# Optimization experiments

Measured on AMD Instinct MI355X. Metric: run time of the kernel, lower is better.

Reference implementation:

```python
import jax, jax.numpy as jnp
import numpy as np

B = 524288   # particles
H = 128      # hidden_size
E = 64       # embed_dim
NT = 512     # num trajectories
IN = 16 + 9 + E  # fc1 input dim = 89
EPS = 1e-6


def setup_inputs() -> dict:
    key = jax.random.key(0)
    ks = jax.random.split(key, 12)
    w = lambda k, shp, fan_in: (jax.random.normal(k, shp, dtype=jnp.float32)
                                / np.sqrt(fan_in).astype(np.float32))
    return {
        "F": jax.random.normal(ks[0], (B, 3, 3), dtype=jnp.float32),
        "C": jax.random.normal(ks[1], (B, 3, 3), dtype=jnp.float32),
        "traj_id": 7,
        "latent": jax.random.normal(ks[2], (NT, E), dtype=jnp.float32),
        "W1": w(ks[3], (IN, H), IN), "b1": jnp.zeros((H,), jnp.float32),
        "W2": w(ks[4], (H, H), H),   "b2": jnp.zeros((H,), jnp.float32),
        "W3": w(ks[5], (H, H), H),   "b3": jnp.zeros((H,), jnp.float32),
        "W4": w(ks[6], (H, H), H),   "b4": jnp.zeros((H,), jnp.float32),
        "W5": w(ks[7], (H, H), H),   "b5": jnp.zeros((H,), jnp.float32),
        "W6": w(ks[8], (H, H), H),   "b6": jnp.zeros((H,), jnp.float32),
        "W7": w(ks[9], (H, 9), H),   "b7": jnp.zeros((9,), jnp.float32),
    }


def _strain_features(F):
    # FFt: [B,3,3]; J = clamp(det F); J1 = clamp(F00); sigma: 3 singular values
    FFt = jnp.einsum('bij,bkj->bik', F, F)
    J = jnp.maximum(jnp.linalg.det(F), EPS)
    J1 = jnp.maximum(F[:, 0, 0], EPS)
    sigma = jnp.linalg.svd(F, compute_uv=False)  # descending, like torch.svd
    return jnp.concatenate([
        FFt.reshape(-1, 9),
        jnp.log(J)[:, None], sigma, J[:, None],
        jnp.log(J1)[:, None], J1[:, None],
    ], axis=-1)  # [B,16]


def reference(F, C, traj_id, latent,
              W1, b1, W2, b2, W3, b3, W4, b4, W5, b5, W6, b6, W7, b7):
    strain = _strain_features(F)                                   # [B,16]
    lat = jnp.broadcast_to(latent[traj_id], (F.shape[0], latent.shape[1]))
    x = jnp.concatenate([strain, C.reshape(-1, 9), lat], axis=-1)  # [B,89]
    g = lambda z: jax.nn.gelu(z, approximate=False)  # exact, matches torch GELU
    x = g(x @ W1 + b1)
    x = g(x @ W2 + b2)
    x = g(x @ W3 + b3)
    x = g(x @ W4 + b4)
    x = g(x @ W5 + b5)
    x = g(x @ W6 + b6)
    out = (x @ W7 + b7).reshape(-1, 3, 3)
    return 0.5 * (out + jnp.swapaxes(out, 1, 2))  # symmetric stress [B,3,3]
```

## Files before the change

### kernel.cpp

```cpp
#include <hip/hip_runtime.h>
#include <hip/hip_bf16.h>
#include <math.h>

#define BPART   524288
#define NBLK    (BPART / 256)
#define W7_OFF  98304
#define WB_N    102400
#define BIAS_N  800
#define PREP_N  (WB_N + BIAS_N)

typedef __bf16 bf16x8 __attribute__((ext_vector_type(8)));
typedef float  f32x16 __attribute__((ext_vector_type(16)));
typedef float  f32x4  __attribute__((ext_vector_type(4)));
typedef float  f32x2  __attribute__((ext_vector_type(2)));
typedef unsigned u32x4 __attribute__((ext_vector_type(4)));

#define MFMA __builtin_amdgcn_mfma_f32_32x32x16_bf16
#define UNROLL _Pragma("unroll")

__device__ __forceinline__ unsigned short f2bf(float f) {
  union { float f; unsigned u; } v; v.f = f;
  unsigned r = v.u + 0x7fffu + ((v.u >> 16) & 1u);
  return (unsigned short)(r >> 16);
}
__device__ __forceinline__ unsigned pack_bf16(float a, float b) {
  unsigned ua = __builtin_bit_cast(unsigned, a) + 0x8000u;
  unsigned ub = __builtin_bit_cast(unsigned, b) + 0x8000u;
  return __builtin_amdgcn_perm(ub, ua, 0x07060302u);
}

__device__ __forceinline__ int sigma(int n) {
  int c = ((n >> 5) << 2) | ((n >> 3) & 3);
  return ((c >> 1) << 4) | (((n >> 2) & 1) << 3) | ((c & 1) << 2) | (n & 3);
}

__device__ __forceinline__ f32x2 pk_mul(f32x2 a, f32x2 b) {
  f32x2 d; asm("v_pk_mul_f32 %0, %1, %2" : "=v"(d) : "v"(a), "v"(b)); return d;
}
__device__ __forceinline__ f32x2 pk_fma(f32x2 a, f32x2 b, f32x2 c) {
  f32x2 d; asm("v_pk_fma_f32 %0, %1, %2, %3" : "=v"(d) : "v"(a), "v"(b), "v"(c)); return d;
}
__device__ __forceinline__ f32x2 gelu2(f32x2 z) {
  const f32x2 c1 = {0.1029432f, 0.1029432f};
  const f32x2 c0 = {2.30220818f, 2.30220818f};
  f32x2 z2 = pk_mul(z, z);
  f32x2 t  = pk_fma(z2, c1, c0);
  f32x2 yp = pk_mul(z, t);
  float e0 = __builtin_amdgcn_exp2f(-yp.x);
  float e1 = __builtin_amdgcn_exp2f(-yp.y);
  float r0 = __builtin_amdgcn_rcpf(e0 + 1.0f);
  float r1 = __builtin_amdgcn_rcpf(e1 + 1.0f);
  f32x2 g; g.x = z.x * r0; g.y = z.y * r1;
  return g;
}
__device__ __forceinline__ void cp16(const void* g, void* l) {
  __builtin_amdgcn_global_load_lds(
      (const __attribute__((address_space(1))) void*)g,
      (__attribute__((address_space(3))) void*)l, 16, 0, 0);
}

__global__ void prep_weights(
    const float* __restrict__ W1, const float* __restrict__ W2,
    const float* __restrict__ W3, const float* __restrict__ W4,
    const float* __restrict__ W5, const float* __restrict__ W6,
    const float* __restrict__ W7,
    const float* __restrict__ b1, const float* __restrict__ b2,
    const float* __restrict__ b3, const float* __restrict__ b4,
    const float* __restrict__ b5, const float* __restrict__ b6,
    const float* __restrict__ b7,
    unsigned short* __restrict__ wsb, float* __restrict__ wsf)
{
  int idx = blockIdx.x * 256 + threadIdx.x;
  if (idx < WB_N) {
    unsigned short v = 0;
    if (idx < W7_OFF) {
      int l = idx >> 14;
      int o = idx & 16383;
      int n = o >> 7, e = o & 127;
      int k = (((e >> 3) ^ (n & 7)) << 3) | (e & 7);
      int sn = sigma(n);
      const float* W = (l==0)?W1:(l==1)?W2:(l==2)?W3:(l==3)?W4:(l==4)?W5:W6;
      float x = (l == 0) ? ((k < 89) ? W[k*128 + sn] : 0.0f)
                         : W[k*128 + sn];
      v = f2bf(x);
    } else {
      int o = idx - W7_OFF;
      int n = o >> 7, e = o & 127;
      int k = (((e >> 3) ^ (n & 7)) << 3) | (e & 7);
      int sn = sigma(n);
      v = (sn < 9) ? f2bf(W7[k*9 + sn]) : (unsigned short)0;
    }
    wsb[idx] = v;
  } else if (idx < PREP_N) {
    int r = idx - WB_N;
    float x;
    if (r < 768) {
      int l = r >> 7, n = r & 127;
      const float* bb = (l==0)?b1:(l==1)?b2:(l==2)?b3:(l==3)?b4:(l==4)?b5:b6;
      x = bb[sigma(n)];
    } else {
      int n = r - 768;
      int sn = sigma(n);
      x = (sn < 9) ? b7[sn] : 0.0f;
    }
    wsf[r] = x;
  }
}

#define MFMA_PAIR(WPTR, BLS, T0, NKK)                                         \
  UNROLL                                                                      \
  for (int kk = 0; kk < (NKK); ++kk) {                                        \
    bf16x8 x_ = __builtin_bit_cast(bf16x8, xw[kk]);                           \
    const int ch_ = ((2*kk + lk) ^ x7) << 3;                                  \
    UNROLL                                                                    \
    for (int t_ = 0; t_ < 2; ++t_) {                                          \
      const int tn_ = (T0) + t_;                                              \
      bf16x8 w_ = *(const bf16x8*)&(WPTR)[tn_*4096 + rb0 + ch_];              \
      if (kk == 0) {                                                          \
        f32x16 cf_;                                                           \
        UNROLL                                                                \
        for (int qq = 0; qq < 4; ++qq) {                                      \
          f32x4 b4_ = *(const f32x4*)&(BLS)[tn_*32 + qq*8 + lk*4];            \
          cf_[4*qq+0] = b4_[0]; cf_[4*qq+1] = b4_[1];                         \
          cf_[4*qq+2] = b4_[2]; cf_[4*qq+3] = b4_[3];                         \
        }                                                                     \
        acc[tn_] = MFMA(w_, x_, cf_, 0, 0, 0);                                \
      } else {                                                                \
        acc[tn_] = MFMA(w_, x_, acc[tn_], 0, 0, 0);                           \
      }                                                                       \
    }                                                                         \
  }

#define MFMA_LAYER(WPTR, NKK)                                                 \
  {                                                                           \
    const unsigned short* wp_ = (WPTR);                                       \
    const float* bls_ = (const float*)((const char*)wp_ + 32768);             \
    MFMA_PAIR(wp_, bls_, 0, NKK)                                              \
    MFMA_PAIR(wp_, bls_, 2, NKK)                                              \
  }

#define GELU_EPILOGUE                                                         \
  UNROLL                                                                      \
  for (int c = 0; c < 16; ++c) {                                              \
    const int tn_ = c >> 2, q_ = c & 3, t_ = c >> 1, h_ = c & 1;              \
    f32x2 za_, zb_;                                                           \
    za_.x = acc[tn_][4*q_+0]; za_.y = acc[tn_][4*q_+1];                       \
    zb_.x = acc[tn_][4*q_+2]; zb_.y = acc[tn_][4*q_+3];                       \
    f32x2 ga_ = gelu2(za_);                                                   \
    f32x2 gb_ = gelu2(zb_);                                                   \
    xw[t_][2*h_ + 0] = pack_bf16(ga_.x, ga_.y);                               \
    xw[t_][2*h_ + 1] = pack_bf16(gb_.x, gb_.y);                               \
  }

#define STAGE_W(LOFF, BUFIDX)                                                 \
  {                                                                           \
    const char* s_ = (const char*)(wst + (LOFF));                             \
    char* d_ = (char*)wbuf[BUFIDX];                                           \
    UNROLL                                                                    \
    for (int i_ = 0; i_ < 4; ++i_)                                            \
      cp16(s_ + i_*8192 + tid*16, d_ + i_*8192 + tid*16);                     \
  }
#define STAGE_B(BOFF, BUFIDX, NT)                                             \
  if (tid < (NT))                                                             \
    cp16((const char*)(wsf + (BOFF)) + tid*16,                                \
         (char*)wbuf[BUFIDX] + 32768 + tid*16);

__global__ __launch_bounds__(512, 4) void stress_mlp(
    const float* __restrict__ F, const float* __restrict__ Cmat,
    const int* __restrict__ traj, const float* __restrict__ latent,
    const unsigned short* __restrict__ wst, const float* __restrict__ wsf,
    float* __restrict__ out)
{
  __shared__ __align__(16) unsigned short wbuf[2][16384 + 256];

  const int tid  = threadIdx.x;
  const int lane = tid & 63;
  const int wid  = tid >> 6;
  const int lm   = lane & 31;
  const int lk   = lane >> 5;
  const int x7   = lm & 7;
  const int rb0  = lm << 7;
  const int pbase = (int)blockIdx.x << 8;
  const int p    = pbase + (wid << 5) + lm;

  STAGE_W(0, 0)
  STAGE_B(0, 0, 32)

  u32x4 xw[8];

  {
    const float* Fp = F + (size_t)p * 9;
    float f[9];
    UNROLL
    for (int i = 0; i < 9; ++i) f[i] = Fp[i];
    float fft[9];
    UNROLL
    for (int i = 0; i < 3; ++i)
      UNROLL
      for (int k = 0; k < 3; ++k)
        fft[i*3+k] = f[i*3]*f[k*3] + f[i*3+1]*f[k*3+1] + f[i*3+2]*f[k*3+2];
    const float* lat = latent + (size_t)traj[0] * 64;

    if (lk == 0) {
      xw[0][0] = pack_bf16(fft[0], fft[1]);
      xw[0][1] = pack_bf16(fft[2], fft[3]);
      xw[0][2] = pack_bf16(fft[4], fft[5]);
      xw[0][3] = pack_bf16(fft[6], fft[7]);
      const float* Cp = Cmat + (size_t)p * 9;
      UNROLL
      for (int i = 0; i < 4; ++i) xw[1][i] = pack_bf16(Cp[2*i], Cp[2*i+1]);
      UNROLL
      for (int t = 0; t < 4; ++t) {
        const float* lb = lat + 7 + 16*t;
        UNROLL
        for (int i = 0; i < 4; ++i) xw[2+t][i] = pack_bf16(lb[2*i], lb[2*i+1]);
      }
    } else {
      float det = f[0]*(f[4]*f[8]-f[5]*f[7]) - f[1]*(f[3]*f[8]-f[5]*f[6])
                + f[2]*(f[3]*f[7]-f[4]*f[6]);
      float J  = fmaxf(det, 1e-6f);
      float J1 = fmaxf(f[0], 1e-6f);
      float a00=fft[0], a01=fft[1], a02=fft[2], a11=fft[4], a12=fft[5], a22=fft[8];
      float q  = (a00+a11+a22) * (1.0f/3.0f);
      float d0 = a00-q, d1 = a11-q, d2 = a22-q;
      float p2 = d0*d0 + d1*d1 + d2*d2 + 2.0f*(a01*a01 + a02*a02 + a12*a12);
      float e0, e1, e2;
      if (p2 < 1e-14f) { e0 = e1 = e2 = q; }
      else {
        float pp  = sqrtf(p2 * (1.0f/6.0f));
        float inv = 1.0f / pp;
        float b00=d0*inv, b11=d1*inv, b22=d2*inv, b01=a01*inv, b02=a02*inv, b12=a12*inv;
        float detb = b00*(b11*b22-b12*b12) - b01*(b01*b22-b12*b02) + b02*(b01*b12-b11*b02);
        float rr = 0.5f * detb;
        rr = fminf(fmaxf(rr, -1.0f), 1.0f);
        float pr = acosf(rr) * (1.0f / (3.0f * 6.2831853071795864f));
        e0 = q + 2.0f*pp*__builtin_amdgcn_cosf(pr);
        e2 = q + 2.0f*pp*__builtin_amdgcn_cosf(pr + (1.0f/3.0f));
        e1 = 3.0f*q - e0 - e2;
      }
      float s0 = sqrtf(fmaxf(e0, 0.f));
      float s1 = sqrtf(fmaxf(e1, 0.f));
      float s2 = sqrtf(fmaxf(e2, 0.f));
      xw[0][0] = pack_bf16(fft[8], logf(J));
      xw[0][1] = pack_bf16(s0, s1);
      xw[0][2] = pack_bf16(s2, J);
      xw[0][3] = pack_bf16(logf(J1), J1);
      float c8 = Cmat[(size_t)p*9 + 8];
      xw[1][0] = pack_bf16(c8, lat[0]);
      xw[1][1] = pack_bf16(lat[1], lat[2]);
      xw[1][2] = pack_bf16(lat[3], lat[4]);
      xw[1][3] = pack_bf16(lat[5], lat[6]);
      UNROLL
      for (int t = 0; t < 3; ++t) {
        const float* lb = lat + 15 + 16*t;
        UNROLL
        for (int i = 0; i < 4; ++i) xw[2+t][i] = pack_bf16(lb[2*i], lb[2*i+1]);
      }
      xw[5][0] = pack_bf16(lat[63], 0.0f);
      xw[5][1] = 0u; xw[5][2] = 0u; xw[5][3] = 0u;
    }
  }

  f32x16 acc[4];

  __syncthreads();
  STAGE_W(1 << 14, 1) STAGE_B(128, 1, 32)
  MFMA_LAYER(wbuf[0], 6)
  GELU_EPILOGUE
  __syncthreads();

  STAGE_W(2 << 14, 0) STAGE_B(256, 0, 32)
  MFMA_LAYER(wbuf[1], 8)
  GELU_EPILOGUE
  __syncthreads();

  STAGE_W(3 << 14, 1) STAGE_B(384, 1, 32)
  MFMA_LAYER(wbuf[0], 8)
  GELU_EPILOGUE
  __syncthreads();

  STAGE_W(4 << 14, 0) STAGE_B(512, 0, 32)
  MFMA_LAYER(wbuf[1], 8)
  GELU_EPILOGUE
  __syncthreads();

  STAGE_W(5 << 14, 1) STAGE_B(640, 1, 32)
  MFMA_LAYER(wbuf[0], 8)
  GELU_EPILOGUE
  __syncthreads();

  {
    const char* s_ = (const char*)(wst + W7_OFF);
    cp16(s_ + tid*16, (char*)wbuf[0] + tid*16);
    STAGE_B(768, 0, 8)
  }
  MFMA_LAYER(wbuf[1], 8)
  GELU_EPILOGUE
  __syncthreads();

  f32x16 a7;
  {
    const unsigned short* wp = wbuf[0];
    const float* bls = (const float*)((const char*)wp + 32768);
    UNROLL
    for (int kk = 0; kk < 8; ++kk) {
      bf16x8 x = __builtin_bit_cast(bf16x8, xw[kk]);
      const int ch = ((2*kk + lk) ^ x7) << 3;
      bf16x8 w = *(const bf16x8*)&wp[rb0 + ch];
      if (kk == 0) {
        f32x16 cf;
        UNROLL
        for (int qq = 0; qq < 4; ++qq) {
          f32x4 b4 = *(const f32x4*)&bls[qq*8 + lk*4];
          cf[4*qq+0] = b4[0]; cf[4*qq+1] = b4[1];
          cf[4*qq+2] = b4[2]; cf[4*qq+3] = b4[3];
        }
        a7 = MFMA(w, x, cf, 0, 0, 0);
      } else {
        a7 = MFMA(w, x, a7, 0, 0, 0);
      }
    }
  }

  float o8 = __shfl_xor(a7[0], 32);
  float* ots = (float*)wbuf[1];
  if (lk == 0) {
    const int row = (wid << 5) + lm;
    float z[9];
    UNROLL
    for (int i = 0; i < 8; ++i) z[i] = a7[i];
    z[8] = o8;
    UNROLL
    for (int rr = 0; rr < 3; ++rr)
      UNROLL
      for (int cc = 0; cc < 3; ++cc)
        ots[row*9 + rr*3 + cc] = 0.5f * (z[rr*3+cc] + z[cc*3+rr]);
  }
  __syncthreads();

  float4* dst = (float4*)(out + (size_t)pbase * 9);
  const float4* srcv = (const float4*)ots;
  UNROLL
  for (int s = tid; s < 576; s += 512) dst[s] = srcv[s];
}

extern "C" void kernel_launch(void* const* d_in, const int* in_sizes, int n_in,
                              void* d_out, int out_size, void* d_ws, size_t ws_size,
                              hipStream_t stream) {
  const float* F   = (const float*)d_in[0];
  const float* C   = (const float*)d_in[1];
  const int*   trj = (const int*)d_in[2];
  const float* lat = (const float*)d_in[3];
  const float* W1  = (const float*)d_in[4];
  const float* b1  = (const float*)d_in[5];
  const float* W2  = (const float*)d_in[6];
  const float* b2  = (const float*)d_in[7];
  const float* W3  = (const float*)d_in[8];
  const float* b3  = (const float*)d_in[9];
  const float* W4  = (const float*)d_in[10];
  const float* b4  = (const float*)d_in[11];
  const float* W5  = (const float*)d_in[12];
  const float* b5  = (const float*)d_in[13];
  const float* W6  = (const float*)d_in[14];
  const float* b6  = (const float*)d_in[15];
  const float* W7  = (const float*)d_in[16];
  const float* b7  = (const float*)d_in[17];

  unsigned short* wsb = (unsigned short*)d_ws;
  float* wsf = (float*)((char*)d_ws + WB_N * 2);

  prep_weights<<<dim3((PREP_N + 255) / 256), dim3(256), 0, stream>>>(
      W1, W2, W3, W4, W5, W6, W7, b1, b2, b3, b4, b5, b6, b7, wsb, wsf);
  stress_mlp<<<dim3(NBLK), dim3(512), 0, stream>>>(
      F, C, trj, lat, wsb, wsf, (float*)d_out);
}
```

Baseline: 283.5 us.

## Process two 32-particle groups per wave to reuse each LDS weight fragment

Each wave now handles 64 particles as two 32-row groups. Every weight fragment read from LDS feeds two MFMAs, which halves LDS weight traffic per particle, and the block shrinks to 256 threads while covering the same 256 particles. The cost is doubled accumulator and activation registers (two sets of 4 f32x16 accumulators) under launch_bounds(256,2), which risks lower occupancy or spills. Fewer waves per block also means fewer threads share the weight staging and the barrier work.

```diff
diff --git a/kernel.cpp b/kernel.cpp
--- a/kernel.cpp
+++ b/kernel.cpp
@@ -107,49 +107,50 @@
   }
 }
 
-#define MFMA_PAIR(WPTR, BLS, T0, NKK)                                         \
-  UNROLL                                                                      \
-  for (int kk = 0; kk < (NKK); ++kk) {                                        \
-    bf16x8 x_ = __builtin_bit_cast(bf16x8, xw[kk]);                           \
-    const int ch_ = ((2*kk + lk) ^ x7) << 3;                                  \
-    UNROLL                                                                    \
-    for (int t_ = 0; t_ < 2; ++t_) {                                          \
-      const int tn_ = (T0) + t_;                                              \
-      bf16x8 w_ = *(const bf16x8*)&(WPTR)[tn_*4096 + rb0 + ch_];              \
-      if (kk == 0) {                                                          \
-        f32x16 cf_;                                                           \
-        UNROLL                                                                \
-        for (int qq = 0; qq < 4; ++qq) {                                      \
-          f32x4 b4_ = *(const f32x4*)&(BLS)[tn_*32 + qq*8 + lk*4];            \
-          cf_[4*qq+0] = b4_[0]; cf_[4*qq+1] = b4_[1];                         \
-          cf_[4*qq+2] = b4_[2]; cf_[4*qq+3] = b4_[3];                         \
-        }                                                                     \
-        acc[tn_] = MFMA(w_, x_, cf_, 0, 0, 0);                                \
-      } else {                                                                \
-        acc[tn_] = MFMA(w_, x_, acc[tn_], 0, 0, 0);                           \
-      }                                                                       \
-    }                                                                         \
-  }
-
 #define MFMA_LAYER(WPTR, NKK)                                                 \
   {                                                                           \
     const unsigned short* wp_ = (WPTR);                                       \
     const float* bls_ = (const float*)((const char*)wp_ + 32768);             \
-    MFMA_PAIR(wp_, bls_, 0, NKK)                                              \
-    MFMA_PAIR(wp_, bls_, 2, NKK)                                              \
+    UNROLL                                                                    \
+    for (int kk = 0; kk < (NKK); ++kk) {                                      \
+      bf16x8 x0_ = __builtin_bit_cast(bf16x8, xw[0][kk]);                     \
+      bf16x8 x1_ = __builtin_bit_cast(bf16x8, xw[1][kk]);                     \
+      const int ch_ = ((2*kk + lk) ^ x7) << 3;                                \
+      UNROLL                                                                  \
+      for (int tn_ = 0; tn_ < 4; ++tn_) {                                     \
+        bf16x8 w_ = *(const bf16x8*)&wp_[tn_*4096 + rb0 + ch_];               \
+        if (kk == 0) {                                                        \
+          f32x16 cf_;                                                         \
+          UNROLL                                                              \
+          for (int qq = 0; qq < 4; ++qq) {                                    \
+            f32x4 b4_ = *(const f32x4*)&bls_[tn_*32 + qq*8 + lk*4];           \
+            cf_[4*qq+0] = b4_[0]; cf_[4*qq+1] = b4_[1];                       \
+            cf_[4*qq+2] = b4_[2]; cf_[4*qq+3] = b4_[3];                       \
+          }                                                                   \
+          acc[0][tn_] = MFMA(w_, x0_, cf_, 0, 0, 0);                          \
+          acc[1][tn_] = MFMA(w_, x1_, cf_, 0, 0, 0);                          \
+        } else {                                                              \
+          acc[0][tn_] = MFMA(w_, x0_, acc[0][tn_], 0, 0, 0);                  \
+          acc[1][tn_] = MFMA(w_, x1_, acc[1][tn_], 0, 0, 0);                  \
+        }                                                                     \
+      }                                                                       \
+    }                                                                         \
   }
 
 #define GELU_EPILOGUE                                                         \
   UNROLL                                                                      \
-  for (int c = 0; c < 16; ++c) {                                              \
-    const int tn_ = c >> 2, q_ = c & 3, t_ = c >> 1, h_ = c & 1;              \
-    f32x2 za_, zb_;                                                           \
-    za_.x = acc[tn_][4*q_+0]; za_.y = acc[tn_][4*q_+1];                       \
-    zb_.x = acc[tn_][4*q_+2]; zb_.y = acc[tn_][4*q_+3];                       \
-    f32x2 ga_ = gelu2(za_);                                                   \
-    f32x2 gb_ = gelu2(zb_);                                                   \
-    xw[t_][2*h_ + 0] = pack_bf16(ga_.x, ga_.y);                               \
-    xw[t_][2*h_ + 1] = pack_bf16(gb_.x, gb_.y);                               \
+  for (int g_ = 0; g_ < 2; ++g_) {                                            \
+    UNROLL                                                                    \
+    for (int c = 0; c < 16; ++c) {                                            \
+      const int tn_ = c >> 2, q_ = c & 3, t_ = c >> 1, h_ = c & 1;            \
+      f32x2 za_, zb_;                                                         \
+      za_.x = acc[g_][tn_][4*q_+0]; za_.y = acc[g_][tn_][4*q_+1];             \
+      zb_.x = acc[g_][tn_][4*q_+2]; zb_.y = acc[g_][tn_][4*q_+3];             \
+      f32x2 ga_ = gelu2(za_);                                                 \
+      f32x2 gb_ = gelu2(zb_);                                                 \
+      xw[g_][t_][2*h_ + 0] = pack_bf16(ga_.x, ga_.y);                         \
+      xw[g_][t_][2*h_ + 1] = pack_bf16(gb_.x, gb_.y);                         \
+    }                                                                         \
   }
 
 #define STAGE_W(LOFF, BUFIDX)                                                 \
@@ -157,15 +158,15 @@
     const char* s_ = (const char*)(wst + (LOFF));                             \
     char* d_ = (char*)wbuf[BUFIDX];                                           \
     UNROLL                                                                    \
-    for (int i_ = 0; i_ < 4; ++i_)                                            \
-      cp16(s_ + i_*8192 + tid*16, d_ + i_*8192 + tid*16);                     \
+    for (int i_ = 0; i_ < 8; ++i_)                                            \
+      cp16(s_ + i_*4096 + tid*16, d_ + i_*4096 + tid*16);                     \
   }
 #define STAGE_B(BOFF, BUFIDX, NT)                                             \
   if (tid < (NT))                                                             \
     cp16((const char*)(wsf + (BOFF)) + tid*16,                                \
          (char*)wbuf[BUFIDX] + 32768 + tid*16);
 
-__global__ __launch_bounds__(512, 4) void stress_mlp(
+__global__ __launch_bounds__(256, 2) void stress_mlp(
     const float* __restrict__ F, const float* __restrict__ Cmat,
     const int* __restrict__ traj, const float* __restrict__ latent,
     const unsigned short* __restrict__ wst, const float* __restrict__ wsf,
@@ -181,87 +182,104 @@
   const int x7   = lm & 7;
   const int rb0  = lm << 7;
   const int pbase = (int)blockIdx.x << 8;
-  const int p    = pbase + (wid << 5) + lm;
 
   STAGE_W(0, 0)
   STAGE_B(0, 0, 32)
 
-  u32x4 xw[8];
+  u32x4 xw[2][8];
 
   {
-    const float* Fp = F + (size_t)p * 9;
-    float f[9];
+    const float* lat = latent + (size_t)traj[0] * 64;
     UNROLL
-    for (int i = 0; i < 9; ++i) f[i] = Fp[i];
-    float fft[9];
-    UNROLL
-    for (int i = 0; i < 3; ++i)
+    for (int g = 0; g < 2; ++g) {
+      const int p = pbase + (wid << 6) + (g << 5) + lm;
+      const float* Fp = F + (size_t)p * 9;
+      float f[9];
       UNROLL
-      for (int k = 0; k < 3; ++k)
-        fft[i*3+k] = f[i*3]*f[k*3] + f[i*3+1]*f[k*3+1] + f[i*3+2]*f[k*3+2];
-    const float* lat = latent + (size_t)traj[0] * 64;
-
-    if (lk == 0) {
-      xw[0][0] = pack_bf16(fft[0], fft[1]);
-      xw[0][1] = pack_bf16(fft[2], fft[3]);
-      xw[0][2] = pack_bf16(fft[4], fft[5]);
-      xw[0][3] = pack_bf16(fft[6], fft[7]);
-      const float* Cp = Cmat + (size_t)p * 9;
+      for (int i = 0; i < 9; ++i) f[i] = Fp[i];
+      float fft[9];
       UNROLL
-      for (int i = 0; i < 4; ++i) xw[1][i] = pack_bf16(Cp[2*i], Cp[2*i+1]);
-      UNROLL
-      for (int t = 0; t < 4; ++t) {
-        const float* lb = lat + 7 + 16*t;
+      for (int i = 0; i < 3; ++i)
         UNROLL
-        for (int i = 0; i < 4; ++i) xw[2+t][i] = pack_bf16(lb[2*i], lb[2*i+1]);
+        for (int k = 0; k < 3; ++k)
+          fft[i*3+k] = f[i*3]*f[k*3] + f[i*3+1]*f[k*3+1] + f[i*3+2]*f[k*3+2];
+
+      if (lk == 0) {
+        xw[g][0][0] = pack_bf16(fft[0], fft[1]);
+        xw[g][0][1] = pack_bf16(fft[2], fft[3]);
+        xw[g][0][2] = pack_bf16(fft[4], fft[5]);
+        xw[g][0][3] = pack_bf16(fft[6], fft[7]);
+        const float* Cp = Cmat + (size_t)p * 9;
+        UNROLL
+        for (int i = 0; i < 4; ++i) xw[g][1][i] = pack_bf16(Cp[2*i], Cp[2*i+1]);
+        if (g == 0) {
+          UNROLL
+          for (int t = 0; t < 4; ++t) {
+            const float* lb = lat + 7 + 16*t;
+            UNROLL
+            for (int i = 0; i < 4; ++i) xw[0][2+t][i] = pack_bf16(lb[2*i], lb[2*i+1]);
+          }
+        } else {
+          UNROLL
+          for (int t = 0; t < 4; ++t) xw[1][2+t] = xw[0][2+t];
+        }
+      } else {
+        float det = f[0]*(f[4]*f[8]-f[5]*f[7]) - f[1]*(f[3]*f[8]-f[5]*f[6])
+                  + f[2]*(f[3]*f[7]-f[4]*f[6]);
+        float J  = fmaxf(det, 1e-6f);
+        float J1 = fmaxf(f[0], 1e-6f);
+        float a00=fft[0], a01=fft[1], a02=fft[2], a11=fft[4], a12=fft[5], a22=fft[8];
+        float q  = (a00+a11+a22) * (1.0f/3.0f);
+        float d0 = a00-q, d1 = a11-q, d2 = a22-q;
+        float p2 = d0*d0 + d1*d1 + d2*d2 + 2.0f*(a01*a01 + a02*a02 + a12*a12);
+        float e0, e1, e2;
+        if (p2 < 1e-14f) { e0 = e1 = e2 = q; }
+        else {
+          float pp  = sqrtf(p2 * (1.0f/6.0f));
+          float inv = 1.0f / pp;
+          float b00=d0*inv, b11=d1*inv, b22=d2*inv, b01=a01*inv, b02=a02*inv, b12=a12*inv;
+          float detb = b00*(b11*b22-b12*b12) - b01*(b01*b22-b12*b02) + b02*(b01*b12-b11*b02);
+          float rr = 0.5f * detb;
+          rr = fminf(fmaxf(rr, -1.0f), 1.0f);
+          float pr = acosf(rr) * (1.0f / (3.0f * 6.2831853071795864f));
+          e0 = q + 2.0f*pp*__builtin_amdgcn_cosf(pr);
+          e2 = q + 2.0f*pp*__builtin_amdgcn_cosf(pr + (1.0f/3.0f));
+          e1 = 3.0f*q - e0 - e2;
+        }
+        float s0 = sqrtf(fmaxf(e0, 0.f));
+        float s1 = sqrtf(fmaxf(e1, 0.f));
+        float s2 = sqrtf(fmaxf(e2, 0.f));
+        xw[g][0][0] = pack_bf16(fft[8], logf(J));
+        xw[g][0][1] = pack_bf16(s0, s1);
+        xw[g][0][2] = pack_bf16(s2, J);
+        xw[g][0][3] = pack_bf16(logf(J1), J1);
+        float c8 = Cmat[(size_t)p*9 + 8];
+        xw[g][1][0] = pack_bf16(c8, lat[0]);
+        if (g == 0) {
+          xw[0][1][1] = pack_bf16(lat[1], lat[2]);
+          xw[0][1][2] = pack_bf16(lat[3], lat[4]);
+          xw[0][1][3] = pack_bf16(lat[5], lat[6]);
+          UNROLL
+          for (int t = 0; t < 3; ++t) {
+            const float* lb = lat + 15 + 16*t;
+            UNROLL
+            for (int i = 0; i < 4; ++i) xw[0][2+t][i] = pack_bf16(lb[2*i], lb[2*i+1]);
+          }
+          xw[0][5][0] = pack_bf16(lat[63], 0.0f);
+          xw[0][5][1] = 0u; xw[0][5][2] = 0u; xw[0][5][3] = 0u;
+        } else {
+          xw[1][1][1] = xw[0][1][1];
+          xw[1][1][2] = xw[0][1][2];
+          xw[1][1][3] = xw[0][1][3];
+          UNROLL
+          for (int t = 0; t < 3; ++t) xw[1][2+t] = xw[0][2+t];
+          xw[1][5] = xw[0][5];
+        }
       }
-    } else {
-      float det = f[0]*(f[4]*f[8]-f[5]*f[7]) - f[1]*(f[3]*f[8]-f[5]*f[6])
-                + f[2]*(f[3]*f[7]-f[4]*f[6]);
-      float J  = fmaxf(det, 1e-6f);
-      float J1 = fmaxf(f[0], 1e-6f);
-      float a00=fft[0], a01=fft[1], a02=fft[2], a11=fft[4], a12=fft[5], a22=fft[8];
-      float q  = (a00+a11+a22) * (1.0f/3.0f);
-      float d0 = a00-q, d1 = a11-q, d2 = a22-q;
-      float p2 = d0*d0 + d1*d1 + d2*d2 + 2.0f*(a01*a01 + a02*a02 + a12*a12);
-      float e0, e1, e2;
-      if (p2 < 1e-14f) { e0 = e1 = e2 = q; }
-      else {
-        float pp  = sqrtf(p2 * (1.0f/6.0f));
-        float inv = 1.0f / pp;
-        float b00=d0*inv, b11=d1*inv, b22=d2*inv, b01=a01*inv, b02=a02*inv, b12=a12*inv;
-        float detb = b00*(b11*b22-b12*b12) - b01*(b01*b22-b12*b02) + b02*(b01*b12-b11*b02);
-        float rr = 0.5f * detb;
-        rr = fminf(fmaxf(rr, -1.0f), 1.0f);
-        float pr = acosf(rr) * (1.0f / (3.0f * 6.2831853071795864f));
-        e0 = q + 2.0f*pp*__builtin_amdgcn_cosf(pr);
-        e2 = q + 2.0f*pp*__builtin_amdgcn_cosf(pr + (1.0f/3.0f));
-        e1 = 3.0f*q - e0 - e2;
-      }
-      float s0 = sqrtf(fmaxf(e0, 0.f));
-      float s1 = sqrtf(fmaxf(e1, 0.f));
-      float s2 = sqrtf(fmaxf(e2, 0.f));
-      xw[0][0] = pack_bf16(fft[8], logf(J));
-      xw[0][1] = pack_bf16(s0, s1);
-      xw[0][2] = pack_bf16(s2, J);
-      xw[0][3] = pack_bf16(logf(J1), J1);
-      float c8 = Cmat[(size_t)p*9 + 8];
-      xw[1][0] = pack_bf16(c8, lat[0]);
-      xw[1][1] = pack_bf16(lat[1], lat[2]);
-      xw[1][2] = pack_bf16(lat[3], lat[4]);
-      xw[1][3] = pack_bf16(lat[5], lat[6]);
-      UNROLL
-      for (int t = 0; t < 3; ++t) {
-        const float* lb = lat + 15 + 16*t;
-        UNROLL
-        for (int i = 0; i < 4; ++i) xw[2+t][i] = pack_bf16(lb[2*i], lb[2*i+1]);
-      }
-      xw[5][0] = pack_bf16(lat[63], 0.0f);
-      xw[5][1] = 0u; xw[5][2] = 0u; xw[5][3] = 0u;
     }
   }
 
-  f32x16 acc[4];
+  f32x16 acc[2][4];
 
   __syncthreads();
   STAGE_W(1 << 14, 1) STAGE_B(128, 1, 32)
@@ -291,20 +309,23 @@
 
   {
     const char* s_ = (const char*)(wst + W7_OFF);
-    cp16(s_ + tid*16, (char*)wbuf[0] + tid*16);
+    UNROLL
+    for (int i_ = 0; i_ < 2; ++i_)
+      cp16(s_ + i_*4096 + tid*16, (char*)wbuf[0] + i_*4096 + tid*16);
     STAGE_B(768, 0, 8)
   }
   MFMA_LAYER(wbuf[1], 8)
   GELU_EPILOGUE
   __syncthreads();
 
-  f32x16 a7;
+  f32x16 a7[2];
   {
     const unsigned short* wp = wbuf[0];
     const float* bls = (const float*)((const char*)wp + 32768);
     UNROLL
     for (int kk = 0; kk < 8; ++kk) {
-      bf16x8 x = __builtin_bit_cast(bf16x8, xw[kk]);
+      bf16x8 x0 = __builtin_bit_cast(bf16x8, xw[0][kk]);
+      bf16x8 x1 = __builtin_bit_cast(bf16x8, xw[1][kk]);
       const int ch = ((2*kk + lk) ^ x7) << 3;
       bf16x8 w = *(const bf16x8*)&wp[rb0 + ch];
       if (kk == 0) {
@@ -315,33 +336,38 @@
           cf[4*qq+0] = b4[0]; cf[4*qq+1] = b4[1];
           cf[4*qq+2] = b4[2]; cf[4*qq+3] = b4[3];
         }
-        a7 = MFMA(w, x, cf, 0, 0, 0);
+        a7[0] = MFMA(w, x0, cf, 0, 0, 0);
+        a7[1] = MFMA(w, x1, cf, 0, 0, 0);
       } else {
-        a7 = MFMA(w, x, a7, 0, 0, 0);
+        a7[0] = MFMA(w, x0, a7[0], 0, 0, 0);
+        a7[1] = MFMA(w, x1, a7[1], 0, 0, 0);
       }
     }
   }
 
-  float o8 = __shfl_xor(a7[0], 32);
   float* ots = (float*)wbuf[1];
-  if (lk == 0) {
-    const int row = (wid << 5) + lm;
-    float z[9];
-    UNROLL
-    for (int i = 0; i < 8; ++i) z[i] = a7[i];
-    z[8] = o8;
-    UNROLL
-    for (int rr = 0; rr < 3; ++rr)
+  UNROLL
+  for (int g = 0; g < 2; ++g) {
+    float o8 = __shfl_xor(a7[g][0], 32);
+    if (lk == 0) {
+      const int row = (wid << 6) + (g << 5) + lm;
+      float z[9];
       UNROLL
-      for (int cc = 0; cc < 3; ++cc)
-        ots[row*9 + rr*3 + cc] = 0.5f * (z[rr*3+cc] + z[cc*3+rr]);
+      for (int i = 0; i < 8; ++i) z[i] = a7[g][i];
+      z[8] = o8;
+      UNROLL
+      for (int rr = 0; rr < 3; ++rr)
+        UNROLL
+        for (int cc = 0; cc < 3; ++cc)
+          ots[row*9 + rr*3 + cc] = 0.5f * (z[rr*3+cc] + z[cc*3+rr]);
+    }
   }
   __syncthreads();
 
   float4* dst = (float4*)(out + (size_t)pbase * 9);
   const float4* srcv = (const float4*)ots;
   UNROLL
-  for (int s = tid; s < 576; s += 512) dst[s] = srcv[s];
+  for (int s = tid; s < 576; s += 256) dst[s] = srcv[s];
 }
 
 extern "C" void kernel_launch(void* const* d_in, const int* in_sizes, int n_in,
@@ -371,6 +397,6 @@
 
   prep_weights<<<dim3((PREP_N + 255) / 256), dim3(256), 0, stream>>>(
       W1, W2, W3, W4, W5, W6, W7, b1, b2, b3, b4, b5, b6, b7, wsb, wsf);
-  stress_mlp<<<dim3(NBLK), dim3(512), 0, stream>>>(
+  stress_mlp<<<dim3(NBLK), dim3(256), 0, stream>>>(
       F, C, trj, lat, wsb, wsf, (float*)d_out);
 }
```

Result: faster. 257.5 us (-9.2%).

## Interleave GELU epilogue of previous layer with next layer's MFMAs

Applied to the files above, without the earlier changes.

Moves each layer's GELU epilogue into the following layer. The activation of accumulator tile G is computed just before the MFMAs that consume its k-chunks, so transcendental VALU work can overlap in-flight matrix instructions instead of running as a separate serial phase. The MFMA issue order is reshuffled so partially ready inputs feed all four output tiles progressively. The cost is more complex scheduling and possible register pressure, since old and new accumulators are live at the same time.

```diff
diff --git a/kernel.cpp b/kernel.cpp
--- a/kernel.cpp
+++ b/kernel.cpp
@@ -107,49 +107,79 @@
   }
 }
 
-#define MFMA_PAIR(WPTR, BLS, T0, NKK)                                         \
+#define MF1(KK, TN, WP, BLS)                                                  \
+  {                                                                           \
+    bf16x8 x_ = __builtin_bit_cast(bf16x8, xw[KK]);                           \
+    const int ch_ = (((2*(KK)) + lk) ^ x7) << 3;                              \
+    bf16x8 w_ = *(const bf16x8*)&(WP)[(TN)*4096 + rb0 + ch_];                 \
+    if ((KK) == 0) {                                                          \
+      f32x16 cf_;                                                             \
+      UNROLL                                                                  \
+      for (int qq = 0; qq < 4; ++qq) {                                        \
+        f32x4 b4_ = *(const f32x4*)&(BLS)[(TN)*32 + qq*8 + lk*4];             \
+        cf_[4*qq+0] = b4_[0]; cf_[4*qq+1] = b4_[1];                           \
+        cf_[4*qq+2] = b4_[2]; cf_[4*qq+3] = b4_[3];                           \
+      }                                                                       \
+      acc[TN] = MFMA(w_, x_, cf_, 0, 0, 0);                                   \
+    } else {                                                                  \
+      acc[TN] = MFMA(w_, x_, acc[TN], 0, 0, 0);                               \
+    }                                                                         \
+  }
+
+#define GELU_Q(G)                                                             \
   UNROLL                                                                      \
-  for (int kk = 0; kk < (NKK); ++kk) {                                        \
-    bf16x8 x_ = __builtin_bit_cast(bf16x8, xw[kk]);                           \
-    const int ch_ = ((2*kk + lk) ^ x7) << 3;                                  \
-    UNROLL                                                                    \
-    for (int t_ = 0; t_ < 2; ++t_) {                                          \
-      const int tn_ = (T0) + t_;                                              \
-      bf16x8 w_ = *(const bf16x8*)&(WPTR)[tn_*4096 + rb0 + ch_];              \
-      if (kk == 0) {                                                          \
-        f32x16 cf_;                                                           \
-        UNROLL                                                                \
-        for (int qq = 0; qq < 4; ++qq) {                                      \
-          f32x4 b4_ = *(const f32x4*)&(BLS)[tn_*32 + qq*8 + lk*4];            \
-          cf_[4*qq+0] = b4_[0]; cf_[4*qq+1] = b4_[1];                         \
-          cf_[4*qq+2] = b4_[2]; cf_[4*qq+3] = b4_[3];                         \
-        }                                                                     \
-        acc[tn_] = MFMA(w_, x_, cf_, 0, 0, 0);                                \
-      } else {                                                                \
-        acc[tn_] = MFMA(w_, x_, acc[tn_], 0, 0, 0);                           \
-      }                                                                       \
-    }                                                                         \
-  }
-
-#define MFMA_LAYER(WPTR, NKK)                                                 \
-  {                                                                           \
-    const unsigned short* wp_ = (WPTR);                                       \
-    const float* bls_ = (const float*)((const char*)wp_ + 32768);             \
-    MFMA_PAIR(wp_, bls_, 0, NKK)                                              \
-    MFMA_PAIR(wp_, bls_, 2, NKK)                                              \
-  }
-
-#define GELU_EPILOGUE                                                         \
-  UNROLL                                                                      \
-  for (int c = 0; c < 16; ++c) {                                              \
-    const int tn_ = c >> 2, q_ = c & 3, t_ = c >> 1, h_ = c & 1;              \
+  for (int cc = 0; cc < 4; ++cc) {                                            \
+    const int c = 4*(G) + cc;                                                 \
+    const int t_ = c >> 1, h_ = c & 1;                                        \
     f32x2 za_, zb_;                                                           \
-    za_.x = acc[tn_][4*q_+0]; za_.y = acc[tn_][4*q_+1];                       \
-    zb_.x = acc[tn_][4*q_+2]; zb_.y = acc[tn_][4*q_+3];                       \
+    za_.x = acc[G][4*cc+0]; za_.y = acc[G][4*cc+1];                           \
+    zb_.x = acc[G][4*cc+2]; zb_.y = acc[G][4*cc+3];                           \
     f32x2 ga_ = gelu2(za_);                                                   \
     f32x2 gb_ = gelu2(zb_);                                                   \
     xw[t_][2*h_ + 0] = pack_bf16(ga_.x, ga_.y);                               \
     xw[t_][2*h_ + 1] = pack_bf16(gb_.x, gb_.y);                               \
+  }
+
+#define FUSED_LAYER(WPTR)                                                     \
+  {                                                                           \
+    const unsigned short* wp_ = (WPTR);                                       \
+    const float* bls_ = (const float*)((const char*)wp_ + 32768);             \
+    GELU_Q(0)                                                                 \
+    MF1(0,0,wp_,bls_) MF1(1,0,wp_,bls_)                                       \
+    GELU_Q(1)                                                                 \
+    MF1(0,1,wp_,bls_) MF1(1,1,wp_,bls_)                                       \
+    MF1(2,0,wp_,bls_) MF1(3,0,wp_,bls_)                                       \
+    MF1(2,1,wp_,bls_) MF1(3,1,wp_,bls_)                                       \
+    GELU_Q(2)                                                                 \
+    MF1(0,2,wp_,bls_) MF1(1,2,wp_,bls_)                                       \
+    MF1(2,2,wp_,bls_) MF1(3,2,wp_,bls_)                                       \
+    MF1(4,0,wp_,bls_) MF1(4,1,wp_,bls_) MF1(4,2,wp_,bls_)                     \
+    MF1(5,0,wp_,bls_) MF1(5,1,wp_,bls_) MF1(5,2,wp_,bls_)                     \
+    GELU_Q(3)                                                                 \
+    MF1(0,3,wp_,bls_) MF1(1,3,wp_,bls_)                                       \
+    MF1(2,3,wp_,bls_) MF1(3,3,wp_,bls_)                                       \
+    MF1(4,3,wp_,bls_) MF1(5,3,wp_,bls_)                                       \
+    MF1(6,0,wp_,bls_) MF1(6,1,wp_,bls_) MF1(6,2,wp_,bls_) MF1(6,3,wp_,bls_)   \
+    MF1(7,0,wp_,bls_) MF1(7,1,wp_,bls_) MF1(7,2,wp_,bls_) MF1(7,3,wp_,bls_)   \
+  }
+
+#define A7S(KK, WP, BLS)                                                      \
+  {                                                                           \
+    bf16x8 x_ = __builtin_bit_cast(bf16x8, xw[KK]);                           \
+    const int ch_ = (((2*(KK)) + lk) ^ x7) << 3;                              \
+    bf16x8 w_ = *(const bf16x8*)&(WP)[rb0 + ch_];                             \
+    if ((KK) == 0) {                                                          \
+      f32x16 cf_;                                                             \
+      UNROLL                                                                  \
+      for (int qq = 0; qq < 4; ++qq) {                                        \
+        f32x4 b4_ = *(const f32x4*)&(BLS)[qq*8 + lk*4];                       \
+        cf_[4*qq+0] = b4_[0]; cf_[4*qq+1] = b4_[1];                           \
+        cf_[4*qq+2] = b4_[2]; cf_[4*qq+3] = b4_[3];                           \
+      }                                                                       \
+      a7 = MFMA(w_, x_, cf_, 0, 0, 0);                                        \
+    } else {                                                                  \
+      a7 = MFMA(w_, x_, a7, 0, 0, 0);                                         \
+    }                                                                         \
   }
 
 #define STAGE_W(LOFF, BUFIDX)                                                 \
@@ -265,28 +295,31 @@
 
   __syncthreads();
   STAGE_W(1 << 14, 1) STAGE_B(128, 1, 32)
-  MFMA_LAYER(wbuf[0], 6)
-  GELU_EPILOGUE
+  {
+    const unsigned short* wp_ = wbuf[0];
+    const float* bls_ = (const float*)((const char*)wp_ + 32768);
+    UNROLL
+    for (int kk = 0; kk < 6; ++kk) {
+      MF1(kk, 0, wp_, bls_) MF1(kk, 1, wp_, bls_)
+      MF1(kk, 2, wp_, bls_) MF1(kk, 3, wp_, bls_)
+    }
+  }
   __syncthreads();
 
   STAGE_W(2 << 14, 0) STAGE_B(256, 0, 32)
-  MFMA_LAYER(wbuf[1], 8)
-  GELU_EPILOGUE
+  FUSED_LAYER(wbuf[1])
   __syncthreads();
 
   STAGE_W(3 << 14, 1) STAGE_B(384, 1, 32)
-  MFMA_LAYER(wbuf[0], 8)
-  GELU_EPILOGUE
+  FUSED_LAYER(wbuf[0])
   __syncthreads();
 
   STAGE_W(4 << 14, 0) STAGE_B(512, 0, 32)
-  MFMA_LAYER(wbuf[1], 8)
-  GELU_EPILOGUE
+  FUSED_LAYER(wbuf[1])
   __syncthreads();
 
   STAGE_W(5 << 14, 1) STAGE_B(640, 1, 32)
-  MFMA_LAYER(wbuf[0], 8)
-  GELU_EPILOGUE
+  FUSED_LAYER(wbuf[0])
   __syncthreads();
 
   {
@@ -294,32 +327,21 @@
     cp16(s_ + tid*16, (char*)wbuf[0] + tid*16);
     STAGE_B(768, 0, 8)
   }
-  MFMA_LAYER(wbuf[1], 8)
-  GELU_EPILOGUE
+  FUSED_LAYER(wbuf[1])
   __syncthreads();
 
   f32x16 a7;
   {
-    const unsigned short* wp = wbuf[0];
-    const float* bls = (const float*)((const char*)wp + 32768);
-    UNROLL
-    for (int kk = 0; kk < 8; ++kk) {
-      bf16x8 x = __builtin_bit_cast(bf16x8, xw[kk]);
-      const int ch = ((2*kk + lk) ^ x7) << 3;
-      bf16x8 w = *(const bf16x8*)&wp[rb0 + ch];
-      if (kk == 0) {
-        f32x16 cf;
-        UNROLL
-        for (int qq = 0; qq < 4; ++qq) {
-          f32x4 b4 = *(const f32x4*)&bls[qq*8 + lk*4];
-          cf[4*qq+0] = b4[0]; cf[4*qq+1] = b4[1];
-          cf[4*qq+2] = b4[2]; cf[4*qq+3] = b4[3];
-        }
-        a7 = MFMA(w, x, cf, 0, 0, 0);
-      } else {
-        a7 = MFMA(w, x, a7, 0, 0, 0);
-      }
-    }
+    const unsigned short* wp_ = wbuf[0];
+    const float* bls_ = (const float*)((const char*)wp_ + 32768);
+    GELU_Q(0)
+    A7S(0, wp_, bls_) A7S(1, wp_, bls_)
+    GELU_Q(1)
+    A7S(2, wp_, bls_) A7S(3, wp_, bls_)
+    GELU_Q(2)
+    A7S(4, wp_, bls_) A7S(5, wp_, bls_)
+    GELU_Q(3)
+    A7S(6, wp_, bls_) A7S(7, wp_, bls_)
   }
 
   float o8 = __shfl_xor(a7[0], 32);
@@ -333,8 +355,8 @@
     UNROLL
     for (int rr = 0; rr < 3; ++rr)
       UNROLL
-      for (int cc = 0; cc < 3; ++cc)
-        ots[row*9 + rr*3 + cc] = 0.5f * (z[rr*3+cc] + z[cc*3+rr]);
+      for (int cc2 = 0; cc2 < 3; ++cc2)
+        ots[row*9 + rr*3 + cc2] = 0.5f * (z[rr*3+cc2] + z[cc2*3+rr]);
   }
   __syncthreads();
 
```

Result: slower. 298.1 us (+5.2%).
